# Performance work log

Measured on AMD Instinct MI355X. Metric: run time of the kernel, lower is better.

## Reference

```python
import jax, jax.numpy as jnp
import numpy as np

B, SQ, SE, H, NH = 2, 2048, 2048, 1024, 16
HD = H // NH  # 64

def setup_inputs() -> dict:
    key = jax.random.key(0)
    ks = jax.random.split(key, 8)
    s = 1.0 / np.sqrt(H)
    return {
        "hidden_states": jax.random.normal(ks[0], (B, SQ, H), jnp.float32),
        "encoder_hidden_states": jax.random.normal(ks[1], (B, SE, H), jnp.float32),
        "attention_mask": jnp.zeros((B, 1, 1, SQ + SE), jnp.float32),
        "Wq": jax.random.normal(ks[2], (H, H), jnp.float32) * s,
        "bq": jnp.zeros((H,), jnp.float32),
        "Wk": jax.random.normal(ks[3], (H, H), jnp.float32) * s,
        "bk": jnp.zeros((H,), jnp.float32),
        "Wv": jax.random.normal(ks[4], (H, H), jnp.float32) * s,
        "bv": jnp.zeros((H,), jnp.float32),
    }

def _split_heads(x):
    # [B, S, H] -> [B, NH, S, HD]
    b, s, _ = x.shape
    return x.reshape(b, s, NH, HD).transpose(0, 2, 1, 3)

def reference(hidden_states, encoder_hidden_states, attention_mask, Wq, bq, Wk, bk, Wv, bv):
    # Q from self tokens; K,V from concat(self, encoder) along sequence
    all_hs = jnp.concatenate([hidden_states, encoder_hidden_states], axis=1)  # [B, SQ+SE, H]
    q = _split_heads(hidden_states @ Wq + bq)   # [B, NH, SQ, HD]
    k = _split_heads(all_hs @ Wk + bk)          # [B, NH, SKV, HD]
    v = _split_heads(all_hs @ Wv + bv)          # [B, NH, SKV, HD]
    scores = jnp.einsum('bhqd,bhkd->bhqk', q, k) / jnp.sqrt(jnp.float32(HD))
    scores = scores + attention_mask            # additive mask, broadcast [B,1,1,SKV]
    probs = jax.nn.softmax(scores, axis=-1)     # dropout p=0 (eval)
    ctx = jnp.einsum('bhqk,bhkd->bhqd', probs, v)
    ctx = ctx.transpose(0, 2, 1, 3).reshape(hidden_states.shape[0], hidden_states.shape[1], H)
    return ctx
```

## Files before the change

### kernel.cpp

```cpp
#include <hip/hip_runtime.h>
#include <hip/hip_bf16.h>
#include <stdint.h>


typedef __attribute__((ext_vector_type(8))) short short8;
typedef __attribute__((ext_vector_type(4))) float f32x4;
typedef __attribute__((ext_vector_type(4))) unsigned short us4;

typedef __attribute__((ext_vector_type(8), may_alias)) short short8a;
typedef __attribute__((ext_vector_type(4), may_alias)) float f32x4a;
typedef __attribute__((may_alias)) unsigned long long u64a;
typedef __attribute__((may_alias)) float floata;

#define MEMBAR() asm volatile("" ::: "memory")
#define DEV static __device__ __forceinline__

DEV unsigned short f2bf(float f) {
  unsigned int u = __builtin_bit_cast(unsigned int, f);
  u += 0x7fffu + ((u >> 16) & 1u);
  return (unsigned short)(u >> 16);
}

DEV float exp2_(float x) {
#if __has_builtin(__builtin_amdgcn_exp2f)
  return __builtin_amdgcn_exp2f(x);
#else
  float r; asm("v_exp_f32 %0, %1" : "=v"(r) : "v"(x)); return r;
#endif
}

DEV unsigned int cvtpk_bf16(float lo, float hi) {
  unsigned int r;
  asm("v_cvt_pk_bf16_f32 %0, %1, %2" : "=v"(r) : "v"(lo), "v"(hi));
  return r;
}

DEV void g2lds16(const void* g, void* l) {
  __builtin_amdgcn_global_load_lds((const __attribute__((address_space(1))) void*)g,
                                   (__attribute__((address_space(3))) void*)l, 16, 0, 0);
}

__global__ __launch_bounds__(256) void convert_allhs(const float* __restrict__ hid,
                                                     const float* __restrict__ enc,
                                                     unsigned short* __restrict__ ah) {
  int idx = blockIdx.x * 256 + threadIdx.x;
  const int perB = 4096 * 256;
  int b = idx / perB, r = idx - b * perB;
  int s = r >> 8, c4 = r & 255;
  const float* srcrow = (s < 2048) ? hid + (size_t)(b * 2048 + s) * 1024
                                   : enc + (size_t)(b * 2048 + (s - 2048)) * 1024;
  f32x4 v = *(const f32x4*)(srcrow + c4 * 4);
  us4 o;
  o[0] = f2bf(v[0]); o[1] = f2bf(v[1]); o[2] = f2bf(v[2]); o[3] = f2bf(v[3]);
  *(us4*)(ah + (size_t)idx * 4) = o;
}

__global__ __launch_bounds__(256) void premul_mask(const float* __restrict__ m,
                                                   float* __restrict__ o) {
  int i = blockIdx.x * 256 + threadIdx.x;
  o[i] = m[i] * 1.4426950408889634f;
}

__global__ __launch_bounds__(256) void transpose_w3(const float* __restrict__ Wq,
                                                    const float* __restrict__ Wk,
                                                    const float* __restrict__ Wv,
                                                    unsigned short* __restrict__ WtBase) {
  __shared__ unsigned short t[64][65];
  const int z = blockIdx.z;
  const float* W = (z == 0) ? Wq : (z == 1) ? Wk : Wv;
  unsigned short* Wt = WtBase + (size_t)z * 1048576;
  int k0 = blockIdx.y * 64, n0 = blockIdx.x * 64;
  int tid = threadIdx.x;
#pragma unroll
  for (int rep = 0; rep < 16; rep++) {
    int idx = rep * 256 + tid;
    int kk = idx >> 6, nn = idx & 63;
    t[kk][nn] = f2bf(W[(size_t)(k0 + kk) * 1024 + n0 + nn]);
  }
  __syncthreads();
#pragma unroll
  for (int rep = 0; rep < 16; rep++) {
    int idx = rep * 256 + tid;
    int nn = idx >> 6, kk = idx & 63;
    Wt[(size_t)(n0 + nn) * 1024 + k0 + kk] = t[kk][nn];
  }
}

__global__ __launch_bounds__(256) void gemm_all(const unsigned short* __restrict__ WTQ,
                                                const unsigned short* __restrict__ WTK,
                                                const unsigned short* __restrict__ WTV,
                                                const unsigned short* __restrict__ AH,
                                                const float* __restrict__ bq,
                                                const float* __restrict__ bk,
                                                const float* __restrict__ bv,
                                                unsigned short* __restrict__ Qout,
                                                unsigned short* __restrict__ Kout,
                                                unsigned short* __restrict__ Vout,
                                                float qscale) {
  __shared__ unsigned short ldsA[128 * 32];
  __shared__ unsigned short ldsB[128 * 32];

  int id = blockIdx.x;
  int f2 = (id & 7) * 160 + (id >> 3);

  const unsigned short *A, *Bm;
  const float* bias;
  unsigned short* outb;
  int S, mode, r0, c0;
  float osc = 1.0f;
  if (f2 < 256) {
    int t = f2;
    int b = t >> 7; t &= 127;
    c0 = (t & 15) * 128; r0 = (t >> 4) * 128;
    A = WTQ; Bm = AH + (size_t)b * 4194304; bias = bq;
    outb = Qout + (size_t)b * 2097152; S = 2048; mode = 0; osc = qscale;
  } else if (f2 < 768) {
    int t = f2 - 256;
    int b = t >> 8; t &= 255;
    c0 = (t & 31) * 128; r0 = (t >> 5) * 128;
    A = WTK; Bm = AH + (size_t)b * 4194304; bias = bk;
    outb = Kout + (size_t)b * 4194304; S = 4096; mode = 0;
  } else {
    int t = f2 - 768;
    int b = t >> 8; t &= 255;
    c0 = (t & 7) * 128; r0 = (t >> 3) * 128;
    A = AH + (size_t)b * 4194304; Bm = WTV; bias = bv;
    outb = Vout + (size_t)b * 4194304; S = 4096; mode = 1;
  }

  const int tid = threadIdx.x, w = tid >> 6, l = tid & 63;
  const int wr = w >> 1, wc = w & 1;
  const int lrow = l >> 2, lk = (l & 3) * 8;
  const int lc = l & 15, g = l >> 4;

  f32x4 acc[4][4];
#pragma unroll
  for (int i = 0; i < 4; i++)
#pragma unroll
    for (int j = 0; j < 4; j++) acc[i][j] = (f32x4){0.f, 0.f, 0.f, 0.f};

  for (int k0 = 0; k0 < 1024; k0 += 32) {
#pragma unroll
    for (int t = 0; t < 2; t++) {
      const int tt = w * 2 + t;
      g2lds16(A + (size_t)(r0 + tt * 16 + lrow) * 1024 + k0 + lk, (char*)ldsA + tt * 1024);
      g2lds16(Bm + (size_t)(c0 + tt * 16 + lrow) * 1024 + k0 + lk, (char*)ldsB + tt * 1024);
    }
    __syncthreads();
    short8 af[4], bf[4];
#pragma unroll
    for (int f = 0; f < 4; f++) {
      af[f] = *(const short8*)((const char*)ldsA + (wr * 64 + f * 16 + lc) * 64 + g * 16);
      bf[f] = *(const short8*)((const char*)ldsB + (wc * 64 + f * 16 + lc) * 64 + g * 16);
    }
#pragma unroll
    for (int fr = 0; fr < 4; fr++)
#pragma unroll
      for (int fc = 0; fc < 4; fc++)
        acc[fr][fc] = __builtin_amdgcn_mfma_f32_16x16x32_bf16(af[fr], bf[fc], acc[fr][fc], 0, 0, 0);
    __syncthreads();
  }

#pragma unroll
  for (int fr = 0; fr < 4; fr++) {
    int rb = r0 + wr * 64 + fr * 16 + g * 4;
    float bv4[4];
    if (mode == 0) {
#pragma unroll
      for (int i = 0; i < 4; i++) bv4[i] = bias[rb + i];
    }
#pragma unroll
    for (int fc = 0; fc < 4; fc++) {
      int c = c0 + wc * 64 + fc * 16 + lc;
      float bc = (mode == 0) ? 0.f : bias[c];
      us4 pk;
#pragma unroll
      for (int i = 0; i < 4; i++) {
        float v = (acc[fr][fc][i] + (mode == 0 ? bv4[i] : bc)) * osc;
        pk[i] = f2bf(v);
      }
      size_t addr;
      if (mode == 0) addr = ((size_t)(rb >> 6) * S + c) * 64 + (rb & 63);
      else           addr = (size_t)c * S + rb;
      *(us4*)(outb + addr) = pk;
    }
  }
}

__global__ __launch_bounds__(256) void attn_kernel(const unsigned short* __restrict__ Q,
                                                   const unsigned short* __restrict__ K,
                                                   const unsigned short* __restrict__ Vt,
                                                   const float* __restrict__ mask2,
                                                   float* __restrict__ out) {
  __shared__ __align__(16) char ldsK[2][8192];
  __shared__ __align__(16) char ldsV[2][8192];
  __shared__ __align__(16) char plds[16384];

  int flat = blockIdx.x + 32 * (blockIdx.y + 16 * blockIdx.z);
  int xc = flat & 7, tt = flat >> 3;
  int f2 = xc * 64 + (tt & 63) + (tt >> 6) * 512;
  const int qt = f2 & 31, h = (f2 >> 5) & 15, b = f2 >> 9;

  const int tid = threadIdx.x, w = tid >> 6, l = tid & 63;
  const int rg = w & 1, kh = w >> 1;
  const int lc = l & 15, g = l >> 4;

  const unsigned short* Qb = Q + ((size_t)(b * 16 + h) * 2048) * 64;
  const unsigned short* Kb = K + ((size_t)((b * 16 + h) * 4096 + kh * 2048)) * 64;
  const unsigned short* Vb = Vt + ((size_t)(b * 16 + h) * 64) * 4096 + kh * 2048;
  const float* mk = mask2 + (size_t)b * 4096 + kh * 2048;
  const int sq0 = qt * 64 + rg * 32;

  const int srow = l >> 3;
  const int schunk = (l & 7) ^ srow;

  short8 qf[2][2];
#pragma unroll
  for (int c2 = 0; c2 < 2; c2++)
#pragma unroll
    for (int hh = 0; hh < 2; hh++)
      qf[c2][hh] = *(const short8*)(Qb + (size_t)(sq0 + c2 * 16 + lc) * 64 + hh * 32 + g * 8);

  short8 ones;
#pragma unroll
  for (int i = 0; i < 8; i++) ones[i] = (short)0x3f80;

  f32x4 ctx[2][4];
#pragma unroll
  for (int c2 = 0; c2 < 2; c2++)
#pragma unroll
    for (int df = 0; df < 4; df++) ctx[c2][df] = (f32x4){0.f, 0.f, 0.f, 0.f};
  f32x4 lsacc[2];
  lsacc[0] = (f32x4){0.f, 0.f, 0.f, 0.f};
  lsacc[1] = (f32x4){0.f, 0.f, 0.f, 0.f};

  char* kbase = ldsK[kh];
  char* vbase = ldsV[kh];
  char* pwave = plds + w * 4096;
  const int swz = (lc & 7) << 4;

  {
    short8 kreg[4], vreg[4];
#pragma unroll
    for (int c = 0; c < 4; c++) {
      int r = (rg * 4 + c) * 8 + srow;
      kreg[c] = *(const short8*)(Kb + (size_t)r * 64 + schunk * 8);
      vreg[c] = *(const short8*)(Vb + (size_t)r * 4096 + schunk * 8);
    }
#pragma unroll
    for (int c = 0; c < 4; c++) {
      *(short8a*)(kbase + (rg * 4 + c) * 1024 + l * 16) = kreg[c];
      *(short8a*)(vbase + (rg * 4 + c) * 1024 + l * 16) = vreg[c];
    }
  }
  __syncthreads();

  for (int t = 0; t < 32; t++) {
    const int s0 = t * 64;

    f32x4 mvv[4];
#pragma unroll
    for (int f = 0; f < 4; f++)
      mvv[f] = *(const f32x4*)(mk + s0 + f * 16 + g * 4);

    short8 kreg[4], vreg[4];
    if (t < 31) {
#pragma unroll
      for (int c = 0; c < 4; c++) {
        int r = (rg * 4 + c) * 8 + srow;
        kreg[c] = *(const short8*)(Kb + (size_t)(s0 + 64 + r) * 64 + schunk * 8);
        vreg[c] = *(const short8*)(Vb + (size_t)r * 4096 + (s0 + 64) + schunk * 8);
      }
    }

#pragma unroll
    for (int f = 0; f < 4; f++) {
      short8 k0 = *(const short8*)(kbase + (f * 16 + lc) * 128 + ((g ^ (lc & 7)) << 4));
      short8 k1 = *(const short8*)(kbase + (f * 16 + lc) * 128 + (((4 + g) ^ (lc & 7)) << 4));
#pragma unroll
      for (int c2 = 0; c2 < 2; c2++) {
        f32x4 z = __builtin_amdgcn_mfma_f32_16x16x32_bf16(k0, qf[c2][0], mvv[f], 0, 0, 0);
        z = __builtin_amdgcn_mfma_f32_16x16x32_bf16(k1, qf[c2][1], z, 0, 0, 0);
        unsigned int lo = cvtpk_bf16(exp2_(z[0]), exp2_(z[1]));
        unsigned int hi = cvtpk_bf16(exp2_(z[2]), exp2_(z[3]));
        int base = lc * 128 + f * 32 + g * 8;
        *(u64a*)(pwave + c2 * 2048 + (base ^ swz)) = ((unsigned long long)hi << 32) | lo;
      }
    }

    MEMBAR();

    short8 pfrag[2][2];
#pragma unroll
    for (int c2 = 0; c2 < 2; c2++)
#pragma unroll
      for (int kk = 0; kk < 2; kk++)
        pfrag[c2][kk] = (short8)*(const short8a*)(pwave + c2 * 2048 + ((lc * 128 + kk * 64 + g * 16) ^ swz));
#pragma unroll
    for (int df = 0; df < 4; df++) {
      short8 v0 = *(const short8*)(vbase + (df * 16 + lc) * 128 + ((g ^ (lc & 7)) << 4));
      short8 v1 = *(const short8*)(vbase + (df * 16 + lc) * 128 + (((4 + g) ^ (lc & 7)) << 4));
#pragma unroll
      for (int c2 = 0; c2 < 2; c2++) {
        ctx[c2][df] = __builtin_amdgcn_mfma_f32_16x16x32_bf16(v0, pfrag[c2][0], ctx[c2][df], 0, 0, 0);
        ctx[c2][df] = __builtin_amdgcn_mfma_f32_16x16x32_bf16(v1, pfrag[c2][1], ctx[c2][df], 0, 0, 0);
      }
    }
#pragma unroll
    for (int c2 = 0; c2 < 2; c2++) {
      lsacc[c2] = __builtin_amdgcn_mfma_f32_16x16x32_bf16(ones, pfrag[c2][0], lsacc[c2], 0, 0, 0);
      lsacc[c2] = __builtin_amdgcn_mfma_f32_16x16x32_bf16(ones, pfrag[c2][1], lsacc[c2], 0, 0, 0);
    }

    __syncthreads();

    if (t < 31) {
#pragma unroll
      for (int c = 0; c < 4; c++) {
        *(short8a*)(kbase + (rg * 4 + c) * 1024 + l * 16) = kreg[c];
        *(short8a*)(vbase + (rg * 4 + c) * 1024 + l * 16) = vreg[c];
      }
      __syncthreads();
    }
  }

  float* mC = (float*)&ldsK[0][0];
  float* lB = (float*)&plds[0];
  if (kh == 1) {
#pragma unroll
    for (int c2 = 0; c2 < 2; c2++) {
      int row = rg * 32 + c2 * 16 + lc;
#pragma unroll
      for (int df = 0; df < 4; df++) {
        int slot = (df * 4 + g) ^ lc;
        *(f32x4a*)(mC + row * 64 + slot * 4) = ctx[c2][df];
      }
      if (g == 0) *(floata*)(lB + row) = lsacc[c2][0];
    }
  }
  __syncthreads();
  if (kh == 0) {
#pragma unroll
    for (int c2 = 0; c2 < 2; c2++) {
      int row = rg * 32 + c2 * 16 + lc;
      float ls = lsacc[c2][0] + *(const floata*)(lB + row);
      float inv = 1.f / ls;
      size_t orow = (size_t)(b * 2048 + qt * 64 + row);
#pragma unroll
      for (int df = 0; df < 4; df++) {
        int slot = (df * 4 + g) ^ lc;
        f32x4 o = (ctx[c2][df] + *(const f32x4a*)(mC + row * 64 + slot * 4)) * inv;
        *(f32x4*)(out + orow * 1024 + h * 64 + df * 16 + g * 4) = o;
      }
    }
  }
}

extern "C" void kernel_launch(void* const* d_in, const int* in_sizes, int n_in,
                              void* d_out, int out_size, void* d_ws, size_t ws_size,
                              hipStream_t stream) {
  const float* hid = (const float*)d_in[0];
  const float* enc = (const float*)d_in[1];
  const float* mask = (const float*)d_in[2];
  const float* Wq = (const float*)d_in[3];
  const float* bq = (const float*)d_in[4];
  const float* Wk = (const float*)d_in[5];
  const float* bk = (const float*)d_in[6];
  const float* Wv = (const float*)d_in[7];
  const float* bv = (const float*)d_in[8];

  unsigned short* ws = (unsigned short*)d_ws;
  unsigned short* WTQ = ws;
  unsigned short* WTK = ws + 1048576;
  unsigned short* WTV = ws + 2097152;
  unsigned short* AH  = ws + 3145728;
  unsigned short* Qb  = ws + 11534336;
  unsigned short* Kb  = ws + 15728640;
  unsigned short* VT  = ws + 24117248;
  float* mask2 = (float*)(ws + 32505856);

  const float QSCALE = 0.18033688011112042f;

  convert_allhs<<<8192, 256, 0, stream>>>(hid, enc, AH);
  premul_mask<<<32, 256, 0, stream>>>(mask, mask2);
  transpose_w3<<<dim3(16, 16, 3), 256, 0, stream>>>(Wq, Wk, Wv, WTQ);

  gemm_all<<<1280, 256, 0, stream>>>(WTQ, WTK, WTV, AH, bq, bk, bv, Qb, Kb, VT, QSCALE);

  attn_kernel<<<dim3(32, 16, 2), 256, 0, stream>>>(Qb, Kb, VT, mask2, (float*)d_out);
}
```

Baseline: 201.2 us.

## Switch attention core to 32x32x16 MFMA with in-register P via permlane32 swap

Rewrites the attention inner loop to use 32x32x16 bf16 MFMA tiles instead of 16x16x32. The exponentiated probabilities are repacked into B-operand fragments with v_permlane32_swap, so they no longer round-trip through LDS. The row sum is accumulated on the VALU rather than with extra MFMAs against a ones vector. This aims to cut LDS traffic and MFMA issue count, at the cost of more VALU adds and higher register pressure from the 16-wide accumulators.

```diff
diff --git a/kernel.cpp b/kernel.cpp
--- a/kernel.cpp
+++ b/kernel.cpp
@@ -5,14 +5,14 @@
 
 typedef __attribute__((ext_vector_type(8))) short short8;
 typedef __attribute__((ext_vector_type(4))) float f32x4;
+typedef __attribute__((ext_vector_type(16))) float f32x16;
 typedef __attribute__((ext_vector_type(4))) unsigned short us4;
+typedef __attribute__((ext_vector_type(4))) unsigned int u32x4;
 
 typedef __attribute__((ext_vector_type(8), may_alias)) short short8a;
 typedef __attribute__((ext_vector_type(4), may_alias)) float f32x4a;
-typedef __attribute__((may_alias)) unsigned long long u64a;
 typedef __attribute__((may_alias)) float floata;
 
-#define MEMBAR() asm volatile("" ::: "memory")
 #define DEV static __device__ __forceinline__
 
 DEV unsigned short f2bf(float f) {
@@ -192,9 +192,7 @@
                                                    const unsigned short* __restrict__ Vt,
                                                    const float* __restrict__ mask2,
                                                    float* __restrict__ out) {
-  __shared__ __align__(16) char ldsK[2][8192];
-  __shared__ __align__(16) char ldsV[2][8192];
-  __shared__ __align__(16) char plds[16384];
+  __shared__ __align__(16) char lds[32768];
 
   int flat = blockIdx.x + 32 * (blockIdx.y + 16 * blockIdx.z);
   int xc = flat & 7, tt = flat >> 3;
@@ -203,7 +201,7 @@
 
   const int tid = threadIdx.x, w = tid >> 6, l = tid & 63;
   const int rg = w & 1, kh = w >> 1;
-  const int lc = l & 15, g = l >> 4;
+  const int lq = l & 31, h2 = l >> 5;
 
   const unsigned short* Qb = Q + ((size_t)(b * 16 + h) * 2048) * 64;
   const unsigned short* Kb = K + ((size_t)((b * 16 + h) * 4096 + kh * 2048)) * 64;
@@ -211,46 +209,36 @@
   const float* mk = mask2 + (size_t)b * 4096 + kh * 2048;
   const int sq0 = qt * 64 + rg * 32;
 
-  const int srow = l >> 3;
-  const int schunk = (l & 7) ^ srow;
-
-  short8 qf[2][2];
-#pragma unroll
-  for (int c2 = 0; c2 < 2; c2++)
-#pragma unroll
-    for (int hh = 0; hh < 2; hh++)
-      qf[c2][hh] = *(const short8*)(Qb + (size_t)(sq0 + c2 * 16 + lc) * 64 + hh * 32 + g * 8);
-
-  short8 ones;
-#pragma unroll
-  for (int i = 0; i < 8; i++) ones[i] = (short)0x3f80;
-
-  f32x4 ctx[2][4];
-#pragma unroll
-  for (int c2 = 0; c2 < 2; c2++)
-#pragma unroll
-    for (int df = 0; df < 4; df++) ctx[c2][df] = (f32x4){0.f, 0.f, 0.f, 0.f};
-  f32x4 lsacc[2];
-  lsacc[0] = (f32x4){0.f, 0.f, 0.f, 0.f};
-  lsacc[1] = (f32x4){0.f, 0.f, 0.f, 0.f};
-
-  char* kbase = ldsK[kh];
-  char* vbase = ldsV[kh];
-  char* pwave = plds + w * 4096;
-  const int swz = (lc & 7) << 4;
+  char* kbase = lds + kh * 8192;
+  char* vbase = lds + 16384 + kh * 8192;
+
+  const int srow8 = l >> 3, slot = l & 7;
+
+  short8 qf[4];
+#pragma unroll
+  for (int ks = 0; ks < 4; ks++)
+    qf[ks] = *(const short8*)(Qb + (size_t)(sq0 + lq) * 64 + ks * 16 + h2 * 8);
+
+  f32x16 ctx[2];
+#pragma unroll
+  for (int d = 0; d < 2; d++)
+#pragma unroll
+    for (int r = 0; r < 16; r++) ctx[d][r] = 0.f;
+  float lsr = 0.f;
 
   {
     short8 kreg[4], vreg[4];
 #pragma unroll
     for (int c = 0; c < 4; c++) {
-      int r = (rg * 4 + c) * 8 + srow;
-      kreg[c] = *(const short8*)(Kb + (size_t)r * 64 + schunk * 8);
-      vreg[c] = *(const short8*)(Vb + (size_t)r * 4096 + schunk * 8);
+      int kr = rg * 32 + c * 8 + srow8;
+      kreg[c] = *(const short8*)(Kb + (size_t)kr * 64 + (slot ^ (kr & 7)) * 8);
+      vreg[c] = *(const short8*)(Vb + (size_t)kr * 4096 + (slot ^ (kr & 7)) * 8);
     }
 #pragma unroll
     for (int c = 0; c < 4; c++) {
-      *(short8a*)(kbase + (rg * 4 + c) * 1024 + l * 16) = kreg[c];
-      *(short8a*)(vbase + (rg * 4 + c) * 1024 + l * 16) = vreg[c];
+      int kr = rg * 32 + c * 8 + srow8;
+      *(short8a*)(kbase + kr * 128 + slot * 16) = kreg[c];
+      *(short8a*)(vbase + kr * 128 + slot * 16) = vreg[c];
     }
   }
   __syncthreads();
@@ -258,101 +246,112 @@
   for (int t = 0; t < 32; t++) {
     const int s0 = t * 64;
 
-    f32x4 mvv[4];
-#pragma unroll
-    for (int f = 0; f < 4; f++)
-      mvv[f] = *(const f32x4*)(mk + s0 + f * 16 + g * 4);
+    f32x4 mv[2][4];
+#pragma unroll
+    for (int sub = 0; sub < 2; sub++)
+#pragma unroll
+      for (int br = 0; br < 4; br++)
+        mv[sub][br] = *(const f32x4*)(mk + s0 + sub * 32 + br * 8 + h2 * 4);
 
     short8 kreg[4], vreg[4];
     if (t < 31) {
 #pragma unroll
       for (int c = 0; c < 4; c++) {
-        int r = (rg * 4 + c) * 8 + srow;
-        kreg[c] = *(const short8*)(Kb + (size_t)(s0 + 64 + r) * 64 + schunk * 8);
-        vreg[c] = *(const short8*)(Vb + (size_t)r * 4096 + (s0 + 64) + schunk * 8);
-      }
-    }
-
-#pragma unroll
-    for (int f = 0; f < 4; f++) {
-      short8 k0 = *(const short8*)(kbase + (f * 16 + lc) * 128 + ((g ^ (lc & 7)) << 4));
-      short8 k1 = *(const short8*)(kbase + (f * 16 + lc) * 128 + (((4 + g) ^ (lc & 7)) << 4));
-#pragma unroll
-      for (int c2 = 0; c2 < 2; c2++) {
-        f32x4 z = __builtin_amdgcn_mfma_f32_16x16x32_bf16(k0, qf[c2][0], mvv[f], 0, 0, 0);
-        z = __builtin_amdgcn_mfma_f32_16x16x32_bf16(k1, qf[c2][1], z, 0, 0, 0);
-        unsigned int lo = cvtpk_bf16(exp2_(z[0]), exp2_(z[1]));
-        unsigned int hi = cvtpk_bf16(exp2_(z[2]), exp2_(z[3]));
-        int base = lc * 128 + f * 32 + g * 8;
-        *(u64a*)(pwave + c2 * 2048 + (base ^ swz)) = ((unsigned long long)hi << 32) | lo;
-      }
-    }
-
-    MEMBAR();
-
-    short8 pfrag[2][2];
-#pragma unroll
-    for (int c2 = 0; c2 < 2; c2++)
-#pragma unroll
-      for (int kk = 0; kk < 2; kk++)
-        pfrag[c2][kk] = (short8)*(const short8a*)(pwave + c2 * 2048 + ((lc * 128 + kk * 64 + g * 16) ^ swz));
-#pragma unroll
-    for (int df = 0; df < 4; df++) {
-      short8 v0 = *(const short8*)(vbase + (df * 16 + lc) * 128 + ((g ^ (lc & 7)) << 4));
-      short8 v1 = *(const short8*)(vbase + (df * 16 + lc) * 128 + (((4 + g) ^ (lc & 7)) << 4));
-#pragma unroll
-      for (int c2 = 0; c2 < 2; c2++) {
-        ctx[c2][df] = __builtin_amdgcn_mfma_f32_16x16x32_bf16(v0, pfrag[c2][0], ctx[c2][df], 0, 0, 0);
-        ctx[c2][df] = __builtin_amdgcn_mfma_f32_16x16x32_bf16(v1, pfrag[c2][1], ctx[c2][df], 0, 0, 0);
-      }
-    }
-#pragma unroll
-    for (int c2 = 0; c2 < 2; c2++) {
-      lsacc[c2] = __builtin_amdgcn_mfma_f32_16x16x32_bf16(ones, pfrag[c2][0], lsacc[c2], 0, 0, 0);
-      lsacc[c2] = __builtin_amdgcn_mfma_f32_16x16x32_bf16(ones, pfrag[c2][1], lsacc[c2], 0, 0, 0);
-    }
+        int kr = rg * 32 + c * 8 + srow8;
+        kreg[c] = *(const short8*)(Kb + (size_t)(s0 + 64 + kr) * 64 + (slot ^ (kr & 7)) * 8);
+        vreg[c] = *(const short8*)(Vb + (size_t)kr * 4096 + (s0 + 64) + (slot ^ (kr & 7)) * 8);
+      }
+    }
+
+    short8 bfr[2][2];
+#pragma unroll
+    for (int sub = 0; sub < 2; sub++) {
+      f32x16 z;
+#pragma unroll
+      for (int br = 0; br < 4; br++)
+#pragma unroll
+        for (int i = 0; i < 4; i++) z[br * 4 + i] = mv[sub][br][i];
+#pragma unroll
+      for (int ks = 0; ks < 4; ks++) {
+        short8 kf = *(const short8*)(kbase + (sub * 32 + lq) * 128 + (((ks * 2 + h2) ^ (lq & 7)) << 4));
+        z = __builtin_amdgcn_mfma_f32_32x32x16_bf16(kf, qf[ks], z, 0, 0, 0);
+      }
+      float p[16];
+#pragma unroll
+      for (int r = 0; r < 16; r++) { p[r] = exp2_(z[r]); lsr += p[r]; }
+      unsigned int X[4], Y[4];
+#pragma unroll
+      for (int br = 0; br < 4; br++) {
+        X[br] = cvtpk_bf16(p[br * 4 + 0], p[br * 4 + 1]);
+        Y[br] = cvtpk_bf16(p[br * 4 + 2], p[br * 4 + 3]);
+      }
+#pragma unroll
+      for (int k2 = 0; k2 < 2; k2++) {
+        unsigned int xd = X[2 * k2], xs = X[2 * k2 + 1];
+        asm("v_permlane32_swap_b32 %0, %1" : "+v"(xd), "+v"(xs));
+        unsigned int yd = Y[2 * k2], ys = Y[2 * k2 + 1];
+        asm("v_permlane32_swap_b32 %0, %1" : "+v"(yd), "+v"(ys));
+        u32x4 packed = (u32x4){xd, yd, xs, ys};
+        bfr[sub][k2] = __builtin_bit_cast(short8, packed);
+      }
+    }
+
+#pragma unroll
+    for (int dsub = 0; dsub < 2; dsub++)
+#pragma unroll
+      for (int sub = 0; sub < 2; sub++)
+#pragma unroll
+        for (int k2 = 0; k2 < 2; k2++) {
+          short8 vf = *(const short8*)(vbase + (dsub * 32 + lq) * 128 +
+                                       (((sub * 4 + k2 * 2 + h2) ^ (lq & 7)) << 4));
+          ctx[dsub] = __builtin_amdgcn_mfma_f32_32x32x16_bf16(vf, bfr[sub][k2], ctx[dsub], 0, 0, 0);
+        }
 
     __syncthreads();
 
     if (t < 31) {
 #pragma unroll
       for (int c = 0; c < 4; c++) {
-        *(short8a*)(kbase + (rg * 4 + c) * 1024 + l * 16) = kreg[c];
-        *(short8a*)(vbase + (rg * 4 + c) * 1024 + l * 16) = vreg[c];
+        int kr = rg * 32 + c * 8 + srow8;
+        *(short8a*)(kbase + kr * 128 + slot * 16) = kreg[c];
+        *(short8a*)(vbase + kr * 128 + slot * 16) = vreg[c];
       }
       __syncthreads();
     }
   }
 
-  float* mC = (float*)&ldsK[0][0];
-  float* lB = (float*)&plds[0];
+  float ls_tot = lsr + __shfl_xor(lsr, 32, 64);
+
+  float* mC = (float*)lds;
+  float* lB = (float*)(lds + 16384);
+  const int q = rg * 32 + lq;
   if (kh == 1) {
 #pragma unroll
-    for (int c2 = 0; c2 < 2; c2++) {
-      int row = rg * 32 + c2 * 16 + lc;
-#pragma unroll
-      for (int df = 0; df < 4; df++) {
-        int slot = (df * 4 + g) ^ lc;
-        *(f32x4a*)(mC + row * 64 + slot * 4) = ctx[c2][df];
-      }
-      if (g == 0) *(floata*)(lB + row) = lsacc[c2][0];
-    }
+    for (int dsub = 0; dsub < 2; dsub++)
+#pragma unroll
+      for (int br = 0; br < 4; br++) {
+        int d0 = dsub * 32 + br * 8 + h2 * 4;
+        f32x4 v = (f32x4){ctx[dsub][br * 4 + 0], ctx[dsub][br * 4 + 1],
+                          ctx[dsub][br * 4 + 2], ctx[dsub][br * 4 + 3]};
+        *(f32x4a*)((char*)mC + q * 256 + (((d0 >> 2) ^ (q & 15)) << 4)) = v;
+      }
+    if (h2 == 0) *(floata*)(lB + q) = ls_tot;
   }
   __syncthreads();
   if (kh == 0) {
-#pragma unroll
-    for (int c2 = 0; c2 < 2; c2++) {
-      int row = rg * 32 + c2 * 16 + lc;
-      float ls = lsacc[c2][0] + *(const floata*)(lB + row);
-      float inv = 1.f / ls;
-      size_t orow = (size_t)(b * 2048 + qt * 64 + row);
-#pragma unroll
-      for (int df = 0; df < 4; df++) {
-        int slot = (df * 4 + g) ^ lc;
-        f32x4 o = (ctx[c2][df] + *(const f32x4a*)(mC + row * 64 + slot * 4)) * inv;
-        *(f32x4*)(out + orow * 1024 + h * 64 + df * 16 + g * 4) = o;
-      }
-    }
+    float inv = 1.f / (ls_tot + *(const floata*)(lB + q));
+    size_t orow = (size_t)(b * 2048 + qt * 64 + q);
+#pragma unroll
+    for (int dsub = 0; dsub < 2; dsub++)
+#pragma unroll
+      for (int br = 0; br < 4; br++) {
+        int d0 = dsub * 32 + br * 8 + h2 * 4;
+        f32x4 other = *(const f32x4a*)((char*)mC + q * 256 + (((d0 >> 2) ^ (q & 15)) << 4));
+        f32x4 own = (f32x4){ctx[dsub][br * 4 + 0], ctx[dsub][br * 4 + 1],
+                            ctx[dsub][br * 4 + 2], ctx[dsub][br * 4 + 3]};
+        f32x4 o = (own + other) * inv;
+        *(f32x4*)(out + orow * 1024 + h * 64 + d0) = o;
+      }
   }
 }
 
```

After: 191.4 us. 4.9% less time.
